# Kernel tuning notes

Hardware: AMD Instinct MI355X
Metric: run time of the kernel (lower is better)

The kernel has to match this reference:

```python
import jax, jax.numpy as jnp
import numpy as np

D_MODEL = 1024
N_HEADS = 16
D_HEAD = D_MODEL // N_HEADS
B, T = 2, 2048
EPS = 1e-5


def setup_inputs() -> dict:
    key = jax.random.key(0)
    ks = jax.random.split(key, 5)
    s = 1.0 / np.sqrt(D_MODEL)
    return {
        "x": jax.random.normal(ks[0], (B, T, D_MODEL), dtype=jnp.float32),
        "W_q": jax.random.normal(ks[1], (D_MODEL, D_MODEL), dtype=jnp.float32) * s,
        "W_k": jax.random.normal(ks[2], (D_MODEL, D_MODEL), dtype=jnp.float32) * s,
        "W_v": jax.random.normal(ks[3], (D_MODEL, D_MODEL), dtype=jnp.float32) * s,
        "W_o": jax.random.normal(ks[4], (D_MODEL, D_MODEL), dtype=jnp.float32) * s,
        "gn_weight": jnp.ones((D_MODEL,), dtype=jnp.float32),
        "gn_bias": jnp.zeros((D_MODEL,), dtype=jnp.float32),
    }


def reference(x, W_q, W_k, W_v, W_o, gn_weight, gn_bias):
    b, t, dm = x.shape
    h, dh = N_HEADS, D_HEAD
    # per-head decay factors gamma_i = 1 - 2^(-5-i)
    gammas = 1.0 - 2.0 ** (-5.0 - jnp.arange(h, dtype=jnp.float32))  # [H]

    # projections (torch Linear: y = x @ W.T), split heads -> [B,T,H,Dh]
    q = (x @ W_q.T).reshape(b, t, h, dh)
    k = (x @ W_k.T).reshape(b, t, h, dh)
    v = (x @ W_v.T).reshape(b, t, h, dh)

    # causal decay mask D[h,i,j] = gamma_h^(i-j) for i>=j else 0
    idx = jnp.arange(t)
    diff = idx[:, None] - idx[None, :]                      # [T,T]
    pow_ = jnp.maximum(diff, 0).astype(jnp.float32)
    decay = jnp.where(diff >= 0, gammas[:, None, None] ** pow_, 0.0)  # [H,T,T]

    scale = jnp.sqrt(jnp.float32(dh))
    attn = jnp.einsum('bihd,bjhd->bhij', q, k) * decay[None] / scale  # [B,H,T,T]
    y = jnp.einsum('bhij,bjhd->bihd', attn, v)               # [B,T,H,Dh]

    # GroupNorm(n_heads, d_model) over channels-first layout: per (b, head)
    # normalize over (T, d_head)
    mean = y.mean(axis=(1, 3), keepdims=True)
    var = y.var(axis=(1, 3), keepdims=True)
    yn = (y - mean) / jnp.sqrt(var + EPS)
    yn = yn.reshape(b, t, dm) * gn_weight + gn_bias

    return yn @ W_o.T
```

## Files before the change

kernel.cpp:

```cpp
#include <hip/hip_runtime.h>
#include <stdint.h>


#define SEQ 2048

typedef __bf16 bf16x8 __attribute__((ext_vector_type(8)));
typedef float  floatx4 __attribute__((ext_vector_type(4)));
typedef unsigned short ushort4v __attribute__((ext_vector_type(4)));

__device__ __forceinline__ unsigned short f2bf(float f){
    unsigned u = __builtin_bit_cast(unsigned, f);
    u += 0x7fffu + ((u >> 16) & 1u);
    return (unsigned short)(u >> 16);
}

__device__ __forceinline__ void gload_lds16(const void* g, void* l){
    __builtin_amdgcn_global_load_lds(
        (const __attribute__((address_space(1))) unsigned int*)g,
        (__attribute__((address_space(3))) unsigned int*)l, 16, 0, 0);
}

__global__ __launch_bounds__(256)
void cvt_f32_bf16(const float* __restrict__ in, unsigned short* __restrict__ out, int n4){
    int i = blockIdx.x * 256 + threadIdx.x;
    if(i < n4){
        float4 v = ((const float4*)in)[i];
        ushort4v o;
        o[0] = f2bf(v.x); o[1] = f2bf(v.y); o[2] = f2bf(v.z); o[3] = f2bf(v.w);
        *(ushort4v*)&out[(size_t)i*4] = o;
    }
}

__global__ __launch_bounds__(256)
void cvt_w4(const float* __restrict__ w0, const float* __restrict__ w1,
            const float* __restrict__ w2, const float* __restrict__ w3,
            unsigned short* __restrict__ o0, unsigned short* __restrict__ o1,
            unsigned short* __restrict__ o2, unsigned short* __restrict__ o3){
    const int blk = blockIdx.x, seg = blk >> 10;
    const int i = (blk & 1023)*256 + threadIdx.x;
    const float* src = (seg==0)?w0:(seg==1)?w1:(seg==2)?w2:w3;
    unsigned short* dst = (seg==0)?o0:(seg==1)?o1:(seg==2)?o2:o3;
    float4 v = ((const float4*)src)[i];
    ushort4v o;
    o[0] = f2bf(v.x); o[1] = f2bf(v.y); o[2] = f2bf(v.z); o[3] = f2bf(v.w);
    *(ushort4v*)&dst[(size_t)i*4] = o;
}

__global__ __launch_bounds__(256, 3)
void gemm_qkv(const unsigned short* __restrict__ A,
              const unsigned short* __restrict__ Wq,
              const unsigned short* __restrict__ Wk,
              const unsigned short* __restrict__ Wv,
              unsigned short* __restrict__ Qo,
              unsigned short* __restrict__ Ko,
              unsigned short* __restrict__ Vo)
{
    __shared__ unsigned short As[128*32];
    __shared__ unsigned short Bs[128*32];
    const int tid  = threadIdx.x;
    const int w    = tid >> 6, lane = tid & 63, q = lane >> 4, cl = lane & 15;
    const int i0   = blockIdx.x * 128;
    const int ysel = blockIdx.y;
    int mode, n0;
    const unsigned short* Bw;
    unsigned short* O;
    if(ysel < 8)      { mode = 0; Bw = Wq; O = Qo; n0 = ysel*128; }
    else if(ysel < 16){ mode = 1; Bw = Wk; O = Ko; n0 = (ysel-8)*128; }
    else              { mode = 2; Bw = Wv; O = Vo; n0 = (ysel-16)*128; }
    const int wm = (w & 1) * 64, wn = (w >> 1) * 64;

    floatx4 acc[4][4];
    #pragma unroll
    for(int a=0;a<4;a++)
        #pragma unroll
        for(int b=0;b<4;b++) acc[a][b] = (floatx4)(0.0f);

    const int srow = lane >> 2;
    const int soff = (lane & 3) * 16;

    for(int k0 = 0; k0 < 1024; k0 += 32){
        __syncthreads();
        #pragma unroll
        for(int t=0;t<2;t++){
            const int ra = (w*2 + t) * 16;
            gload_lds16((const char*)A  + ((size_t)(i0 + ra + srow)*1024 + k0)*2 + soff,
                        (char*)&As[ra*32]);
            gload_lds16((const char*)Bw + ((size_t)(n0 + ra + srow)*1024 + k0)*2 + soff,
                        (char*)&Bs[ra*32]);
        }
        __syncthreads();

        bf16x8 af[4], bfr[4];
        #pragma unroll
        for(int mi=0;mi<4;mi++) af[mi]  = *(const bf16x8*)&As[(wm + mi*16 + cl)*32 + q*8];
        #pragma unroll
        for(int ni=0;ni<4;ni++) bfr[ni] = *(const bf16x8*)&Bs[(wn + ni*16 + cl)*32 + q*8];
        #pragma unroll
        for(int mi=0;mi<4;mi++)
            #pragma unroll
            for(int ni=0;ni<4;ni++)
                acc[mi][ni] = __builtin_amdgcn_mfma_f32_16x16x32_bf16(af[mi], bfr[ni], acc[mi][ni], 0, 0, 0);
    }

    #pragma unroll
    for(int mi=0;mi<4;mi++)
        #pragma unroll
        for(int ni=0;ni<4;ni++){
            const int gi = i0 + wm + mi*16 + q*4;
            const int gn = n0 + wn + ni*16 + cl;
            const int h = gn >> 6, d = gn & 63;
            const float lgh = log2f(1.0f - exp2f(-5.0f - (float)h));
            if(mode == 2){
                const int b = gi >> 11, t = gi & 2047;
                ushort4v o;
                #pragma unroll
                for(int r=0;r<4;r++) o[r] = f2bf(acc[mi][ni][r]);
                *(ushort4v*)&Vo[(((size_t)(b*16 + h))*64 + d)*2048 + t] = o;
            } else {
                #pragma unroll
                for(int r=0;r<4;r++){
                    const int i = gi + r, b = i >> 11, t = i & 2047;
                    const float sc = (mode == 0) ? exp2f((float)t * lgh) * 0.125f
                                                 : exp2f(-(float)t * lgh);
                    O[(((size_t)(b*16 + h))*2048 + t)*64 + d] = f2bf(acc[mi][ni][r] * sc);
                }
            }
        }
}

__global__ __launch_bounds__(256, 2)
void retention(const unsigned short* __restrict__ Q,
               const unsigned short* __restrict__ K,
               const unsigned short* __restrict__ VT,
               float* __restrict__ Y0, float* __restrict__ Y1)
{
    __shared__ unsigned short Ks[64*64];
    __shared__ unsigned short Vs[64*64];
    __shared__ unsigned short Ss[4][32*64];

    const int tid = threadIdx.x;
    const int w = tid >> 6, lane = tid & 63, q = lane >> 4, cl = lane & 15;
    const int s = blockIdx.x >> 3, x = blockIdx.x & 7;
    const int bh = blockIdx.y;
    const int wm = w * 32;
    const int l3 = lane >> 3, l7 = lane & 7;
    const int c8 = l7 ^ l3;
    const int cl7 = cl & 7;

    int segbt[2], segjb[2], segje[2], nseg;
    if(s == 0){ nseg = 2;
        segbt[0] = x;     segjb[0] = 0;      segje[0] = 2*x + 2;
        segbt[1] = 15-x;  segjb[1] = 0;      segje[1] = 15 - 2*x;
    } else { nseg = 1;
        segbt[0] = 15-x;  segjb[0] = 15-2*x; segje[0] = 32 - 2*x;
    }

    for(int seg = 0; seg < nseg; seg++){
        const int bt = segbt[seg], jb = segjb[seg], je = segje[seg];
        const int i0 = bt * 128;

        bf16x8 qf[2][2];
        #pragma unroll
        for(int mi=0;mi<2;mi++)
            #pragma unroll
            for(int kk=0;kk<2;kk++)
                qf[mi][kk] = *(const bf16x8*)(Q + ((size_t)bh*SEQ + i0 + wm + mi*16 + cl)*64 + kk*32 + q*8);

        floatx4 Yacc[2][4];
        #pragma unroll
        for(int a=0;a<2;a++)
            #pragma unroll
            for(int b=0;b<4;b++) Yacc[a][b] = (floatx4)(0.0f);

        for(int jt = jb; jt < je; jt++){
            const int j0 = jt * 64;
            __syncthreads();
            #pragma unroll
            for(int t=0;t<2;t++){
                const int r = w*16 + t*8 + l3;
                gload_lds16((const char*)K  + (((size_t)bh*SEQ + j0 + r)*64 + c8*8)*2,
                            (char*)&Ks[(w*16 + t*8)*64]);
                gload_lds16((const char*)VT + (((size_t)bh*64 + r)*SEQ + j0 + c8*8)*2,
                            (char*)&Vs[(w*16 + t*8)*64]);
            }
            __syncthreads();

            floatx4 S[2][4];
            #pragma unroll
            for(int a=0;a<2;a++)
                #pragma unroll
                for(int b=0;b<4;b++) S[a][b] = (floatx4)(0.0f);
            #pragma unroll
            for(int kk=0;kk<2;kk++){
                #pragma unroll
                for(int ni=0;ni<4;ni++){
                    bf16x8 bk = *(const bf16x8*)&Ks[(ni*16 + cl)*64 + (((kk*4+q) ^ cl7))*8];
                    S[0][ni] = __builtin_amdgcn_mfma_f32_16x16x32_bf16(qf[0][kk], bk, S[0][ni], 0,0,0);
                    S[1][ni] = __builtin_amdgcn_mfma_f32_16x16x32_bf16(qf[1][kk], bk, S[1][ni], 0,0,0);
                }
            }

            const bool need_mask = (jt >= 2*bt);
            unsigned short* SsW = Ss[w];
            #pragma unroll
            for(int mi=0;mi<2;mi++)
                #pragma unroll
                for(int ni=0;ni<4;ni++)
                    #pragma unroll
                    for(int r=0;r<4;r++){
                        const int row = mi*16 + q*4 + r;
                        float v = S[mi][ni][r];
                        if(need_mask){
                            const int ii = i0 + wm + row;
                            const int jj = j0 + ni*16 + cl;
                            if(ii < jj) v = 0.0f;
                        }
                        SsW[row*64 + (((ni*2 + (cl>>3)) ^ (row & 7))*8) + cl7] = f2bf(v);
                    }
            asm volatile("s_waitcnt lgkmcnt(0)" ::: "memory");

            #pragma unroll
            for(int kk=0;kk<2;kk++){
                const int ch = ((kk*4+q) ^ cl7)*8;
                bf16x8 as0 = *(const bf16x8*)&SsW[( 0 + cl)*64 + ch];
                bf16x8 as1 = *(const bf16x8*)&SsW[(16 + cl)*64 + ch];
                #pragma unroll
                for(int nt=0;nt<4;nt++){
                    bf16x8 bv = *(const bf16x8*)&Vs[(nt*16 + cl)*64 + ch];
                    Yacc[0][nt] = __builtin_amdgcn_mfma_f32_16x16x32_bf16(as0, bv, Yacc[0][nt], 0,0,0);
                    Yacc[1][nt] = __builtin_amdgcn_mfma_f32_16x16x32_bf16(as1, bv, Yacc[1][nt], 0,0,0);
                }
            }
        }

        #pragma unroll
        for(int mi=0;mi<2;mi++)
            #pragma unroll
            for(int nt=0;nt<4;nt++){
                const int gi = i0 + wm + mi*16 + q*4;
                const int gd = nt*16 + cl;
                #pragma unroll
                for(int r=0;r<4;r++){
                    if(s == 0)
                        Y0[((size_t)bh*SEQ + gi + r)*64 + gd] = Yacc[mi][nt][r];
                    else
                        Y1[((size_t)bh*1024 + gi + r - 1024)*64 + gd] = Yacc[mi][nt][r];
                }
            }
    }
}

__global__ __launch_bounds__(256)
void gn_stats(const float* __restrict__ Y0, const float* __restrict__ Y1,
              float* __restrict__ st){
    const int g = blockIdx.x >> 3;
    const int s8 = blockIdx.x & 7;
    const float4* p0 = (const float4*)(Y0 + (size_t)g*131072 + (size_t)s8*16384);
    float s1 = 0.f, s2 = 0.f;
    #pragma unroll
    for(int it=0; it<16; it++){
        float4 v = p0[it*256 + threadIdx.x];
        s1 += v.x + v.y + v.z + v.w;
        s2 += v.x*v.x + v.y*v.y + v.z*v.z + v.w*v.w;
    }
    if(s8 >= 4){
        const float4* p1 = (const float4*)(Y1 + (size_t)g*65536 + (size_t)(s8-4)*16384);
        #pragma unroll
        for(int it=0; it<16; it++){
            float4 v0 = p0[it*256 + threadIdx.x];
            (void)v0;
            float4 v = p1[it*256 + threadIdx.x];
            s1 += v.x + v.y + v.z + v.w;
            s2 += v.x*v.x + v.y*v.y + v.z*v.z + v.w*v.w;
        }
    }
    #pragma unroll
    for(int o=32;o>0;o>>=1){ s1 += __shfl_down(s1,o); s2 += __shfl_down(s2,o); }
    __shared__ float r1[4], r2[4];
    const int w = threadIdx.x >> 6, lane = threadIdx.x & 63;
    if(lane == 0){ r1[w] = s1; r2[w] = s2; }
    __syncthreads();
    if(threadIdx.x == 0){
        atomicAdd(&st[g*2+0], r1[0]+r1[1]+r1[2]+r1[3]);
        atomicAdd(&st[g*2+1], r2[0]+r2[1]+r2[2]+r2[3]);
    }
}

__global__ __launch_bounds__(256)
void gn_stats2(const float* __restrict__ Y0, const float* __restrict__ Y1,
               float* __restrict__ st){
    const int g = blockIdx.x >> 3;
    const int s8 = blockIdx.x & 7;
    const float4* p0 = (const float4*)(Y0 + (size_t)g*131072 + (size_t)s8*16384);
    const float4* p1 = (s8 >= 4) ? (const float4*)(Y1 + (size_t)g*65536 + (size_t)(s8-4)*16384) : nullptr;
    float s1 = 0.f, s2 = 0.f;
    #pragma unroll
    for(int it=0; it<16; it++){
        float4 v = p0[it*256 + threadIdx.x];
        if(p1){
            float4 u = p1[it*256 + threadIdx.x];
            v.x += u.x; v.y += u.y; v.z += u.z; v.w += u.w;
        }
        s1 += v.x + v.y + v.z + v.w;
        s2 += v.x*v.x + v.y*v.y + v.z*v.z + v.w*v.w;
    }
    #pragma unroll
    for(int o=32;o>0;o>>=1){ s1 += __shfl_down(s1,o); s2 += __shfl_down(s2,o); }
    __shared__ float r1[4], r2[4];
    const int w = threadIdx.x >> 6, lane = threadIdx.x & 63;
    if(lane == 0){ r1[w] = s1; r2[w] = s2; }
    __syncthreads();
    if(threadIdx.x == 0){
        atomicAdd(&st[g*2+0], r1[0]+r1[1]+r1[2]+r1[3]);
        atomicAdd(&st[g*2+1], r2[0]+r2[1]+r2[2]+r2[3]);
    }
}

__global__ __launch_bounds__(256)
void gn_norm(const float* __restrict__ Y0, const float* __restrict__ Y1,
             const float* __restrict__ st,
             const float* __restrict__ gw, const float* __restrict__ gb,
             unsigned short* __restrict__ Out){
    const int e4 = blockIdx.x*256 + threadIdx.x;
    float4 v = ((const float4*)Y0)[e4];
    const int e = e4 * 4;
    const int g = e >> 17;
    const int t = (e >> 6) & 2047;
    const int d = e & 63;
    if(t >= 1024){
        const size_t i1 = (((size_t)g*1024 + (t-1024))*64 + d) >> 2;
        float4 u = ((const float4*)Y1)[i1];
        v.x += u.x; v.y += u.y; v.z += u.z; v.w += u.w;
    }
    const int h = g & 15, b = g >> 4;
    const float mean = st[g*2+0] * (1.0f/131072.0f);
    const float var  = st[g*2+1] * (1.0f/131072.0f) - mean*mean;
    const float inv  = rsqrtf(var + 1e-5f);
    const int c = h*64 + d;
    ushort4v o;
    o[0] = f2bf((v.x - mean)*inv*gw[c+0] + gb[c+0]);
    o[1] = f2bf((v.y - mean)*inv*gw[c+1] + gb[c+1]);
    o[2] = f2bf((v.z - mean)*inv*gw[c+2] + gb[c+2]);
    o[3] = f2bf((v.w - mean)*inv*gw[c+3] + gb[c+3]);
    *(ushort4v*)&Out[((size_t)(b*2048 + t))*1024 + c] = o;
}

__global__ __launch_bounds__(256, 3)
void gemm_out(const unsigned short* __restrict__ A,
              const unsigned short* __restrict__ Bw,
              float* __restrict__ O)
{
    __shared__ unsigned short As[128*32];
    __shared__ unsigned short Bs[64*32];
    const int tid = threadIdx.x;
    const int w = tid >> 6, lane = tid & 63, q = lane >> 4, cl = lane & 15;
    const int i0 = blockIdx.x * 128, n0 = blockIdx.y * 64;
    const int wm = (w & 1) * 64, wn = (w >> 1) * 32;

    floatx4 acc[4][2];
    #pragma unroll
    for(int a=0;a<4;a++)
        #pragma unroll
        for(int b=0;b<2;b++) acc[a][b] = (floatx4)(0.0f);

    const int srow = lane >> 2;
    const int soff = (lane & 3) * 16;

    for(int k0 = 0; k0 < 1024; k0 += 32){
        __syncthreads();
        #pragma unroll
        for(int t=0;t<2;t++){
            const int ra = w*32 + t*16;
            gload_lds16((const char*)A + ((size_t)(i0 + ra + srow)*1024 + k0)*2 + soff,
                        (char*)&As[ra*32]);
        }
        gload_lds16((const char*)Bw + ((size_t)(n0 + w*16 + srow)*1024 + k0)*2 + soff,
                    (char*)&Bs[(w*16)*32]);
        __syncthreads();

        bf16x8 af[4], bfr[2];
        #pragma unroll
        for(int mi=0;mi<4;mi++) af[mi]  = *(const bf16x8*)&As[(wm + mi*16 + cl)*32 + q*8];
        #pragma unroll
        for(int ni=0;ni<2;ni++) bfr[ni] = *(const bf16x8*)&Bs[(wn + ni*16 + cl)*32 + q*8];
        #pragma unroll
        for(int mi=0;mi<4;mi++)
            #pragma unroll
            for(int ni=0;ni<2;ni++)
                acc[mi][ni] = __builtin_amdgcn_mfma_f32_16x16x32_bf16(af[mi], bfr[ni], acc[mi][ni], 0, 0, 0);
    }

    #pragma unroll
    for(int mi=0;mi<4;mi++)
        #pragma unroll
        for(int ni=0;ni<2;ni++){
            const int gi = i0 + wm + mi*16 + q*4;
            const int gn = n0 + wn + ni*16 + cl;
            #pragma unroll
            for(int r=0;r<4;r++) O[(size_t)(gi + r)*1024 + gn] = acc[mi][ni][r];
        }
}

extern "C" void kernel_launch(void* const* d_in, const int* in_sizes, int n_in,
                              void* d_out, int out_size, void* d_ws, size_t ws_size,
                              hipStream_t stream){
    const float* x  = (const float*)d_in[0];
    const float* Wq = (const float*)d_in[1];
    const float* Wk = (const float*)d_in[2];
    const float* Wv = (const float*)d_in[3];
    const float* Wo = (const float*)d_in[4];
    const float* gw = (const float*)d_in[5];
    const float* gb = (const float*)d_in[6];

    char* ws = (char*)d_ws;
    unsigned short* xb  = (unsigned short*)(ws + ((size_t) 0<<20));
    unsigned short* wqb = (unsigned short*)(ws + ((size_t) 8<<20));
    unsigned short* wkb = (unsigned short*)(ws + ((size_t)10<<20));
    unsigned short* wvb = (unsigned short*)(ws + ((size_t)12<<20));
    unsigned short* wob = (unsigned short*)(ws + ((size_t)14<<20));
    unsigned short* qb  = (unsigned short*)(ws + ((size_t)16<<20));
    unsigned short* kb  = (unsigned short*)(ws + ((size_t)24<<20));
    unsigned short* vtb = (unsigned short*)(ws + ((size_t)32<<20));
    float*          y0  = (float*)         (ws + ((size_t)40<<20));
    unsigned short* ynb = (unsigned short*)(ws + ((size_t)56<<20));
    float*          y1  = (float*)         (ws + ((size_t) 0<<20));
    float*          st  = (float*)         (ws + ((size_t)64<<20));

    cvt_f32_bf16<<<4096, 256, 0, stream>>>(x, xb, 1048576);
    cvt_w4<<<4096, 256, 0, stream>>>(Wq, Wk, Wv, Wo, wqb, wkb, wvb, wob);

    gemm_qkv<<<dim3(32,24,1), 256, 0, stream>>>(xb, wqb, wkb, wvb, qb, kb, vtb);

    retention<<<dim3(16,32,1), 256, 0, stream>>>(qb, kb, vtb, y0, y1);

    hipMemsetAsync(st, 0, 64*sizeof(float), stream);
    gn_stats2<<<256, 256, 0, stream>>>(y0, y1, st);
    gn_norm<<<4096, 256, 0, stream>>>(y0, y1, st, gw, gb, ynb);

    gemm_out<<<dim3(32,16,1), 256, 0, stream>>>(ynb, wob, (float*)d_out);
}
```

Baseline: 195.6 us.

## Coalesce QKV/retention stores via LDS transposes, merge conversions, drop memset

Merges the two fp32-to-bf16 conversion kernels into one launch that also zeroes the GroupNorm stats buffer, which removes the memset. The QKV GEMM epilogue is staged through swizzled LDS so Q/K/V are written as 16-byte coalesced rows instead of scattered 2-byte stores. The retention kernel swaps MFMA operand order so S and Y come out transposed, giving packed LDS writes, and stores Y in a d-major layout. The GroupNorm stats and norm kernels are rewritten for that layout, with norm transposing through LDS before writing. It also swaps in the native bf16 conversion, which adds more barriers and layout coupling across kernels.

```diff
diff --git a/kernel.cpp b/kernel.cpp
--- a/kernel.cpp
+++ b/kernel.cpp
@@ -9,9 +9,8 @@
 typedef unsigned short ushort4v __attribute__((ext_vector_type(4)));
 
 __device__ __forceinline__ unsigned short f2bf(float f){
-    unsigned u = __builtin_bit_cast(unsigned, f);
-    u += 0x7fffu + ((u >> 16) & 1u);
-    return (unsigned short)(u >> 16);
+    __bf16 h = (__bf16)f;
+    return __builtin_bit_cast(unsigned short, h);
 }
 
 __device__ __forceinline__ void gload_lds16(const void* g, void* l){
@@ -21,29 +20,27 @@
 }
 
 __global__ __launch_bounds__(256)
-void cvt_f32_bf16(const float* __restrict__ in, unsigned short* __restrict__ out, int n4){
-    int i = blockIdx.x * 256 + threadIdx.x;
-    if(i < n4){
-        float4 v = ((const float4*)in)[i];
-        ushort4v o;
-        o[0] = f2bf(v.x); o[1] = f2bf(v.y); o[2] = f2bf(v.z); o[3] = f2bf(v.w);
-        *(ushort4v*)&out[(size_t)i*4] = o;
-    }
-}
-
-__global__ __launch_bounds__(256)
-void cvt_w4(const float* __restrict__ w0, const float* __restrict__ w1,
-            const float* __restrict__ w2, const float* __restrict__ w3,
-            unsigned short* __restrict__ o0, unsigned short* __restrict__ o1,
-            unsigned short* __restrict__ o2, unsigned short* __restrict__ o3){
-    const int blk = blockIdx.x, seg = blk >> 10;
-    const int i = (blk & 1023)*256 + threadIdx.x;
-    const float* src = (seg==0)?w0:(seg==1)?w1:(seg==2)?w2:w3;
-    unsigned short* dst = (seg==0)?o0:(seg==1)?o1:(seg==2)?o2:o3;
+void cvt_all(const float* __restrict__ x,
+             const float* __restrict__ w0, const float* __restrict__ w1,
+             const float* __restrict__ w2, const float* __restrict__ w3,
+             unsigned short* __restrict__ xb,
+             unsigned short* __restrict__ o0, unsigned short* __restrict__ o1,
+             unsigned short* __restrict__ o2, unsigned short* __restrict__ o3,
+             float* __restrict__ st){
+    const int blk = blockIdx.x;
+    if(blk == 0 && threadIdx.x < 128) st[threadIdx.x] = 0.0f;
+    const float* src; unsigned short* dst; size_t i;
+    if(blk < 4096){ src = x; dst = xb; i = (size_t)blk*256 + threadIdx.x; }
+    else {
+        const int seg = (blk - 4096) >> 10;
+        src = seg==0?w0:seg==1?w1:seg==2?w2:w3;
+        dst = seg==0?o0:seg==1?o1:seg==2?o2:o3;
+        i = (size_t)((blk - 4096) & 1023)*256 + threadIdx.x;
+    }
     float4 v = ((const float4*)src)[i];
     ushort4v o;
-    o[0] = f2bf(v.x); o[1] = f2bf(v.y); o[2] = f2bf(v.z); o[3] = f2bf(v.w);
-    *(ushort4v*)&dst[(size_t)i*4] = o;
+    o[0]=f2bf(v.x); o[1]=f2bf(v.y); o[2]=f2bf(v.z); o[3]=f2bf(v.w);
+    *(ushort4v*)&dst[i*4] = o;
 }
 
 __global__ __launch_bounds__(256, 3)
@@ -55,8 +52,9 @@
               unsigned short* __restrict__ Ko,
               unsigned short* __restrict__ Vo)
 {
-    __shared__ unsigned short As[128*32];
-    __shared__ unsigned short Bs[128*32];
+    __shared__ unsigned short smem[8192];
+    unsigned short* As = smem;
+    unsigned short* Bs = smem + 4096;
     const int tid  = threadIdx.x;
     const int w    = tid >> 6, lane = tid & 63, q = lane >> 4, cl = lane & 15;
     const int i0   = blockIdx.x * 128;
@@ -102,30 +100,70 @@
                 acc[mi][ni] = __builtin_amdgcn_mfma_f32_16x16x32_bf16(af[mi], bfr[ni], acc[mi][ni], 0, 0, 0);
     }
 
-    #pragma unroll
-    for(int mi=0;mi<4;mi++)
-        #pragma unroll
-        for(int ni=0;ni<4;ni++){
-            const int gi = i0 + wm + mi*16 + q*4;
-            const int gn = n0 + wn + ni*16 + cl;
-            const int h = gn >> 6, d = gn & 63;
-            const float lgh = log2f(1.0f - exp2f(-5.0f - (float)h));
-            if(mode == 2){
-                const int b = gi >> 11, t = gi & 2047;
-                ushort4v o;
-                #pragma unroll
-                for(int r=0;r<4;r++) o[r] = f2bf(acc[mi][ni][r]);
-                *(ushort4v*)&Vo[(((size_t)(b*16 + h))*64 + d)*2048 + t] = o;
-            } else {
-                #pragma unroll
-                for(int r=0;r<4;r++){
-                    const int i = gi + r, b = i >> 11, t = i & 2047;
-                    const float sc = (mode == 0) ? exp2f((float)t * lgh) * 0.125f
-                                                 : exp2f(-(float)t * lgh);
-                    O[(((size_t)(b*16 + h))*2048 + t)*64 + d] = f2bf(acc[mi][ni][r] * sc);
-                }
-            }
-        }
+    const int b = i0 >> 11;
+    if(mode < 2){
+        for(int p=0;p<2;p++){
+            __syncthreads();
+            if((w & 1) == p){
+                #pragma unroll
+                for(int ni=0;ni<4;ni++){
+                    const int h = (n0 + wn + ni*16) >> 6;
+                    const float lgh = log2f(1.0f - exp2f(-5.0f - (float)h));
+                    const int d = wn + ni*16 + cl, d8 = d >> 3, d7 = d & 7;
+                    #pragma unroll
+                    for(int mi=0;mi<4;mi++)
+                        #pragma unroll
+                        for(int r=0;r<4;r++){
+                            const int trow = mi*16 + q*4 + r;
+                            const int tt = (i0 + p*64 + trow) & 2047;
+                            const float sc = (mode==0) ? exp2f((float)tt*lgh)*0.125f
+                                                       : exp2f(-(float)tt*lgh);
+                            smem[trow*128 + ((d8 ^ (trow & 7))*8) + d7] = f2bf(acc[mi][ni][r]*sc);
+                        }
+                }
+            }
+            __syncthreads();
+            const int trow = tid >> 2, part = tid & 3;
+            const int tt = (i0 + p*64 + trow) & 2047;
+            #pragma unroll
+            for(int k=0;k<4;k++){
+                const int c = k*4 + part;
+                bf16x8 vrow = *(const bf16x8*)&smem[trow*128 + ((c ^ (trow & 7))*8)];
+                const int h = (n0 + c*8) >> 6, dd = (c*8) & 63;
+                *(bf16x8*)&O[(((size_t)(b*16 + h))*2048 + tt)*64 + dd] = vrow;
+            }
+        }
+    } else {
+        for(int p=0;p<2;p++){
+            __syncthreads();
+            if((w >> 1) == p){
+                #pragma unroll
+                for(int ni=0;ni<4;ni++){
+                    const int drow = ni*16 + cl, dr7 = drow & 7;
+                    #pragma unroll
+                    for(int mi=0;mi<4;mi++){
+                        const int t = wm + mi*16 + q*4;
+                        const int c = (t >> 3) ^ dr7;
+                        ushort4v pk;
+                        #pragma unroll
+                        for(int r=0;r<4;r++) pk[r] = f2bf(acc[mi][ni][r]);
+                        *(ushort4v*)&smem[drow*128 + c*8 + (t & 7)] = pk;
+                    }
+                }
+            }
+            __syncthreads();
+            const int drow = tid >> 2, part = tid & 3;
+            const int dg = n0 + p*64 + drow;
+            const int h = dg >> 6, dd = dg & 63;
+            const int tbase = i0 & 2047;
+            #pragma unroll
+            for(int k=0;k<4;k++){
+                const int c = k*4 + part;
+                bf16x8 vrow = *(const bf16x8*)&smem[drow*128 + ((c ^ (drow & 7))*8)];
+                *(bf16x8*)&O[(((size_t)(b*16 + h))*64 + dd)*2048 + tbase + c*8] = vrow;
+            }
+        }
+    }
 }
 
 __global__ __launch_bounds__(256, 2)
@@ -185,50 +223,55 @@
             }
             __syncthreads();
 
-            floatx4 S[2][4];
+            floatx4 St[2][4];
             #pragma unroll
             for(int a=0;a<2;a++)
                 #pragma unroll
-                for(int b=0;b<4;b++) S[a][b] = (floatx4)(0.0f);
+                for(int b=0;b<4;b++) St[a][b] = (floatx4)(0.0f);
             #pragma unroll
             for(int kk=0;kk<2;kk++){
                 #pragma unroll
                 for(int ni=0;ni<4;ni++){
-                    bf16x8 bk = *(const bf16x8*)&Ks[(ni*16 + cl)*64 + (((kk*4+q) ^ cl7))*8];
-                    S[0][ni] = __builtin_amdgcn_mfma_f32_16x16x32_bf16(qf[0][kk], bk, S[0][ni], 0,0,0);
-                    S[1][ni] = __builtin_amdgcn_mfma_f32_16x16x32_bf16(qf[1][kk], bk, S[1][ni], 0,0,0);
+                    bf16x8 ak = *(const bf16x8*)&Ks[(ni*16 + cl)*64 + ((kk*4+q) ^ cl7)*8];
+                    St[0][ni] = __builtin_amdgcn_mfma_f32_16x16x32_bf16(ak, qf[0][kk], St[0][ni], 0,0,0);
+                    St[1][ni] = __builtin_amdgcn_mfma_f32_16x16x32_bf16(ak, qf[1][kk], St[1][ni], 0,0,0);
                 }
             }
 
             const bool need_mask = (jt >= 2*bt);
             unsigned short* SsW = Ss[w];
             #pragma unroll
-            for(int mi=0;mi<2;mi++)
-                #pragma unroll
-                for(int ni=0;ni<4;ni++)
+            for(int mi=0;mi<2;mi++){
+                const int row = mi*16 + cl;
+                const int sw = row & 7;
+                const int ig = i0 + wm + row;
+                #pragma unroll
+                for(int ni=0;ni<4;ni++){
+                    ushort4v pk;
                     #pragma unroll
                     for(int r=0;r<4;r++){
-                        const int row = mi*16 + q*4 + r;
-                        float v = S[mi][ni][r];
+                        float v = St[mi][ni][r];
                         if(need_mask){
-                            const int ii = i0 + wm + row;
-                            const int jj = j0 + ni*16 + cl;
-                            if(ii < jj) v = 0.0f;
+                            const int jg = j0 + ni*16 + q*4 + r;
+                            if(ig < jg) v = 0.0f;
                         }
-                        SsW[row*64 + (((ni*2 + (cl>>3)) ^ (row & 7))*8) + cl7] = f2bf(v);
+                        pk[r] = f2bf(v);
                     }
+                    *(ushort4v*)&SsW[row*64 + (((ni*2 + (q>>1)) ^ sw)*8) + (q&1)*4] = pk;
+                }
+            }
             asm volatile("s_waitcnt lgkmcnt(0)" ::: "memory");
 
             #pragma unroll
             for(int kk=0;kk<2;kk++){
                 const int ch = ((kk*4+q) ^ cl7)*8;
-                bf16x8 as0 = *(const bf16x8*)&SsW[( 0 + cl)*64 + ch];
-                bf16x8 as1 = *(const bf16x8*)&SsW[(16 + cl)*64 + ch];
+                bf16x8 bs0 = *(const bf16x8*)&SsW[( 0 + cl)*64 + ch];
+                bf16x8 bs1 = *(const bf16x8*)&SsW[(16 + cl)*64 + ch];
                 #pragma unroll
                 for(int nt=0;nt<4;nt++){
-                    bf16x8 bv = *(const bf16x8*)&Vs[(nt*16 + cl)*64 + ch];
-                    Yacc[0][nt] = __builtin_amdgcn_mfma_f32_16x16x32_bf16(as0, bv, Yacc[0][nt], 0,0,0);
-                    Yacc[1][nt] = __builtin_amdgcn_mfma_f32_16x16x32_bf16(as1, bv, Yacc[1][nt], 0,0,0);
+                    bf16x8 av = *(const bf16x8*)&Vs[(nt*16 + cl)*64 + ch];
+                    Yacc[0][nt] = __builtin_amdgcn_mfma_f32_16x16x32_bf16(av, bs0, Yacc[0][nt], 0,0,0);
+                    Yacc[1][nt] = __builtin_amdgcn_mfma_f32_16x16x32_bf16(av, bs1, Yacc[1][nt], 0,0,0);
                 }
             }
         }
@@ -237,14 +280,14 @@
         for(int mi=0;mi<2;mi++)
             #pragma unroll
             for(int nt=0;nt<4;nt++){
-                const int gi = i0 + wm + mi*16 + q*4;
-                const int gd = nt*16 + cl;
+                const int ig = i0 + wm + mi*16 + cl;
                 #pragma unroll
                 for(int r=0;r<4;r++){
+                    const int d = nt*16 + q*4 + r;
                     if(s == 0)
-                        Y0[((size_t)bh*SEQ + gi + r)*64 + gd] = Yacc[mi][nt][r];
+                        Y0[((size_t)bh*64 + d)*2048 + ig] = Yacc[mi][nt][r];
                     else
-                        Y1[((size_t)bh*1024 + gi + r - 1024)*64 + gd] = Yacc[mi][nt][r];
+                        Y1[((size_t)bh*64 + d)*1024 + ig - 1024] = Yacc[mi][nt][r];
                 }
             }
     }
@@ -253,26 +296,22 @@
 __global__ __launch_bounds__(256)
 void gn_stats(const float* __restrict__ Y0, const float* __restrict__ Y1,
               float* __restrict__ st){
-    const int g = blockIdx.x >> 3;
-    const int s8 = blockIdx.x & 7;
-    const float4* p0 = (const float4*)(Y0 + (size_t)g*131072 + (size_t)s8*16384);
+    const int g = blockIdx.x >> 3, s8 = blockIdx.x & 7;
+    if(g >= 32) return;
     float s1 = 0.f, s2 = 0.f;
     #pragma unroll
     for(int it=0; it<16; it++){
-        float4 v = p0[it*256 + threadIdx.x];
+        const int idx = it*256 + threadIdx.x;
+        const int dl = idx >> 9;
+        const int t4 = idx & 511;
+        const int drow = g*64 + s8*8 + dl;
+        float4 v = ((const float4*)Y0)[(size_t)drow*512 + t4];
+        if(t4 >= 256){
+            float4 u = ((const float4*)Y1)[(size_t)drow*256 + t4 - 256];
+            v.x += u.x; v.y += u.y; v.z += u.z; v.w += u.w;
+        }
         s1 += v.x + v.y + v.z + v.w;
         s2 += v.x*v.x + v.y*v.y + v.z*v.z + v.w*v.w;
-    }
-    if(s8 >= 4){
-        const float4* p1 = (const float4*)(Y1 + (size_t)g*65536 + (size_t)(s8-4)*16384);
-        #pragma unroll
-        for(int it=0; it<16; it++){
-            float4 v0 = p0[it*256 + threadIdx.x];
-            (void)v0;
-            float4 v = p1[it*256 + threadIdx.x];
-            s1 += v.x + v.y + v.z + v.w;
-            s2 += v.x*v.x + v.y*v.y + v.z*v.z + v.w*v.w;
-        }
     }
     #pragma unroll
     for(int o=32;o>0;o>>=1){ s1 += __shfl_down(s1,o); s2 += __shfl_down(s2,o); }
@@ -287,62 +326,47 @@
 }
 
 __global__ __launch_bounds__(256)
-void gn_stats2(const float* __restrict__ Y0, const float* __restrict__ Y1,
-               float* __restrict__ st){
-    const int g = blockIdx.x >> 3;
-    const int s8 = blockIdx.x & 7;
-    const float4* p0 = (const float4*)(Y0 + (size_t)g*131072 + (size_t)s8*16384);
-    const float4* p1 = (s8 >= 4) ? (const float4*)(Y1 + (size_t)g*65536 + (size_t)(s8-4)*16384) : nullptr;
-    float s1 = 0.f, s2 = 0.f;
-    #pragma unroll
-    for(int it=0; it<16; it++){
-        float4 v = p0[it*256 + threadIdx.x];
-        if(p1){
-            float4 u = p1[it*256 + threadIdx.x];
-            v.x += u.x; v.y += u.y; v.z += u.z; v.w += u.w;
-        }
-        s1 += v.x + v.y + v.z + v.w;
-        s2 += v.x*v.x + v.y*v.y + v.z*v.z + v.w*v.w;
-    }
-    #pragma unroll
-    for(int o=32;o>0;o>>=1){ s1 += __shfl_down(s1,o); s2 += __shfl_down(s2,o); }
-    __shared__ float r1[4], r2[4];
-    const int w = threadIdx.x >> 6, lane = threadIdx.x & 63;
-    if(lane == 0){ r1[w] = s1; r2[w] = s2; }
-    __syncthreads();
-    if(threadIdx.x == 0){
-        atomicAdd(&st[g*2+0], r1[0]+r1[1]+r1[2]+r1[3]);
-        atomicAdd(&st[g*2+1], r2[0]+r2[1]+r2[2]+r2[3]);
-    }
-}
-
-__global__ __launch_bounds__(256)
 void gn_norm(const float* __restrict__ Y0, const float* __restrict__ Y1,
              const float* __restrict__ st,
              const float* __restrict__ gw, const float* __restrict__ gb,
              unsigned short* __restrict__ Out){
-    const int e4 = blockIdx.x*256 + threadIdx.x;
-    float4 v = ((const float4*)Y0)[e4];
-    const int e = e4 * 4;
-    const int g = e >> 17;
-    const int t = (e >> 6) & 2047;
-    const int d = e & 63;
-    if(t >= 1024){
-        const size_t i1 = (((size_t)g*1024 + (t-1024))*64 + d) >> 2;
-        float4 u = ((const float4*)Y1)[i1];
-        v.x += u.x; v.y += u.y; v.z += u.z; v.w += u.w;
-    }
+    __shared__ unsigned short T[64*72];
+    const int g = blockIdx.x >> 5;
+    if(g >= 32) return;
+    const int t0 = (blockIdx.x & 31) * 64;
     const int h = g & 15, b = g >> 4;
     const float mean = st[g*2+0] * (1.0f/131072.0f);
     const float var  = st[g*2+1] * (1.0f/131072.0f) - mean*mean;
     const float inv  = rsqrtf(var + 1e-5f);
-    const int c = h*64 + d;
-    ushort4v o;
-    o[0] = f2bf((v.x - mean)*inv*gw[c+0] + gb[c+0]);
-    o[1] = f2bf((v.y - mean)*inv*gw[c+1] + gb[c+1]);
-    o[2] = f2bf((v.z - mean)*inv*gw[c+2] + gb[c+2]);
-    o[3] = f2bf((v.w - mean)*inv*gw[c+3] + gb[c+3]);
-    *(ushort4v*)&Out[((size_t)(b*2048 + t))*1024 + c] = o;
+    const int tid = threadIdx.x;
+    const bool hi = (t0 >= 1024);
+    #pragma unroll
+    for(int kk=0;kk<4;kk++){
+        const int f4 = kk*256 + tid;
+        const int d = f4 >> 4;
+        const int t4l = f4 & 15;
+        float4 v = ((const float4*)Y0)[(size_t)(g*64 + d)*512 + (t0>>2) + t4l];
+        if(hi){
+            float4 u = ((const float4*)Y1)[(size_t)(g*64 + d)*256 + ((t0-1024)>>2) + t4l];
+            v.x += u.x; v.y += u.y; v.z += u.z; v.w += u.w;
+        }
+        const int c = h*64 + d;
+        const float sc = inv * gw[c];
+        const float bs = gb[c] - mean*sc;
+        const int tl = t4l*4;
+        T[(tl+0)*72 + d] = f2bf(v.x*sc + bs);
+        T[(tl+1)*72 + d] = f2bf(v.y*sc + bs);
+        T[(tl+2)*72 + d] = f2bf(v.z*sc + bs);
+        T[(tl+3)*72 + d] = f2bf(v.w*sc + bs);
+    }
+    __syncthreads();
+    #pragma unroll
+    for(int it=0; it<2; it++){
+        const int idx = it*256 + tid;
+        const int tl = idx >> 3, segp = idx & 7;
+        bf16x8 vrow = *(const bf16x8*)&T[tl*72 + segp*8];
+        *(bf16x8*)&Out[((size_t)(b*2048 + t0 + tl))*1024 + h*64 + segp*8] = vrow;
+    }
 }
 
 __global__ __launch_bounds__(256, 3)
@@ -426,16 +450,14 @@
     float*          y1  = (float*)         (ws + ((size_t) 0<<20));
     float*          st  = (float*)         (ws + ((size_t)64<<20));
 
-    cvt_f32_bf16<<<4096, 256, 0, stream>>>(x, xb, 1048576);
-    cvt_w4<<<4096, 256, 0, stream>>>(Wq, Wk, Wv, Wo, wqb, wkb, wvb, wob);
+    cvt_all<<<8192, 256, 0, stream>>>(x, Wq, Wk, Wv, Wo, xb, wqb, wkb, wvb, wob, st);
 
     gemm_qkv<<<dim3(32,24,1), 256, 0, stream>>>(xb, wqb, wkb, wvb, qb, kb, vtb);
 
     retention<<<dim3(16,32,1), 256, 0, stream>>>(qb, kb, vtb, y0, y1);
 
-    hipMemsetAsync(st, 0, 64*sizeof(float), stream);
-    gn_stats2<<<256, 256, 0, stream>>>(y0, y1, st);
-    gn_norm<<<4096, 256, 0, stream>>>(y0, y1, st, gw, gb, ynb);
+    gn_stats<<<256, 256, 0, stream>>>(y0, y1, st);
+    gn_norm<<<1024, 256, 0, stream>>>(y0, y1, st, gw, gb, ynb);
 
     gemm_out<<<dim3(32,16,1), 256, 0, stream>>>(ynb, wob, (float*)d_out);
 }
```

Result: faster. 188.7 us (-3.5%).
